# Optimization experiments

Measured on AMD Instinct MI355X. Metric: run time of the kernel, lower is better.

Reference implementation:

```python
import jax, jax.numpy as jnp
import numpy as np

NF, NG, NH, NR, HS = 6, 32, 16, 15, 256
NT, NS = 1000, 2000


def _linear_init(k, fan_in, fan_out):
    s = 1.0 / np.sqrt(fan_in)
    kw, kb = jax.random.split(k)
    W = jax.random.uniform(kw, (fan_in, fan_out), minval=-s, maxval=s, dtype=jnp.float32)
    b = jax.random.uniform(kb, (fan_out,), minval=-s, maxval=s, dtype=jnp.float32)
    return W, b


def setup_inputs() -> dict:
    key = jax.random.key(0)
    ks = jax.random.split(key, 12)
    # forcings: Prcp, Evp, T1(min temp), T2(max temp), Rad, Hum; ensure Prcp>=0 and T2>T1
    base = jax.random.normal(ks[0], (NT, NS)) * 10.0
    spread = jax.random.uniform(ks[1], (NT, NS)) * 5.0 + 0.5
    prcp = jax.random.uniform(ks[2], (NT, NS)) * 10.0
    evp = jax.random.uniform(ks[3], (NT, NS)) * 3.0
    rad = jax.random.uniform(ks[4], (NT, NS))
    hum = jax.random.uniform(ks[5], (NT, NS))
    x = jnp.stack([prcp, evp, base - spread, base + spread, rad, hum], axis=-1).astype(jnp.float32)
    xc = jax.random.normal(ks[6], (NS, NG), dtype=jnp.float32)
    W_fc, b_fc = _linear_init(ks[7], NG, HS)
    W_r, b_r = _linear_init(ks[8], HS, NH * (NR + 1))
    W_g, b_g = _linear_init(ks[9], HS, NH * 9)
    W_kin, b_kin = _linear_init(ks[10], 4, HS)
    W_kout, b_kout = _linear_init(ks[11], HS, NH * 1)
    return dict(x=x, xc=xc, W_fc=W_fc, b_fc=b_fc, W_r=W_r, b_r=b_r,
                W_g=W_g, b_g=b_g, W_kin=W_kin, b_kin=b_kin,
                W_kout=W_kout, b_kout=b_kout)


def reference(x, xc, W_fc, b_fc, W_r, b_r, W_g, b_g, W_kin, b_kin, W_kout, b_kout):
    nt, ns, _ = x.shape
    Prcp, Evp, T1, T2 = x[..., 0], x[..., 1], x[..., 2], x[..., 3]
    f = x[..., 2:]                                   # [nt, ns, 4]

    # --- getParam (eval mode: DropMask is identity) ---
    state = xc @ W_fc + b_fc                         # [ns, hs]
    pK = jnp.tanh(f @ W_kin + b_kin + state) @ W_kout + b_kout   # [nt, ns, nh]
    km = jnp.exp(pK)                                 # melt rate per step
    g = jnp.tanh(state)
    pG = g @ W_g + b_g                               # [ns, 9*nh]
    sl = lambda i: pG[..., i * NH:(i + 1) * NH]
    kp = jax.nn.sigmoid(sl(0))
    ks_ = jax.nn.sigmoid(sl(1))
    kd = jax.nn.sigmoid(sl(2))
    gd = jax.nn.sigmoid(sl(3))
    gl = (jax.nn.sigmoid(sl(4)) * 10.0) ** 3
    qb = jax.nn.relu(sl(5)) / 10.0
    ga = jax.nn.softmax(sl(6), axis=-1)
    gi = jnp.clip(sl(7) / 6.0 + 0.5, 0.0, 1.0) / 2.0   # hardsigmoid/2
    ge = jax.nn.relu(sl(8))

    # one-peak routing weights over nr lags: [nr, ns, nh], sums to 1 over lag
    pR = (g @ W_r + b_r).reshape(ns, NH, NR + 1)
    loc = jax.nn.sigmoid(pR[..., 0]) * NR            # peak location in [0, nr]
    lags = jnp.arange(NR, dtype=x.dtype)
    wR = jax.nn.softmax(pR[..., 1:] - (lags - loc[..., None]) ** 2, axis=-1)
    paramR = jnp.transpose(wR, (2, 0, 1))            # [nr, ns, nh]

    # --- divideP: split precip into snow / liquid by the fraction of [T1,T2] above 0C ---
    vL = jnp.clip(T2 / jnp.maximum(T2 - T1, 1e-6), 0.0, 1.0)
    Pl = (Prcp * vL)[..., None]                      # [nt, ns, 1]
    Ps = (Prcp * (1.0 - vL))[..., None]
    Ev = Evp[..., None]

    # --- bucket.step recurrence over time via scan ---
    def step(carry, inp):
        Sf, Ss, Sd = carry
        ps, pl, ev, kmt = inp
        Sf1 = Sf + ps                                # snow bucket
        qf = jnp.minimum(Sf1, kmt)                   # melt
        Sf2 = Sf1 - qf
        Pin = pl + qf                                # liquid input
        H = jax.nn.relu(Ss + Pin * (1.0 - gi) - ev * ge)   # shallow bucket
        qp = jax.nn.relu(H - gl) * kp                # saturation-excess quick flow
        qo = jnp.minimum(H, gl) * ks_                # shallow drainage
        Ss2 = H - qp - qo
        D = Sd + Pin * gi + qo * gd                  # deep bucket
        qd = D * kd + qb                             # baseflow
        Sd2 = D * (1.0 - kd)
        qTot = qp + qo * (1.0 - gd) + qd             # qp + qs + qd
        return (Sf2, Ss2, Sd2), qTot

    z = jnp.zeros((ns, NH), dtype=x.dtype)
    _, qTot = jax.lax.scan(step, (z, z, z), (Ps, Pl, Ev, km))   # [nt, ns, nh]

    # --- windowed routing convolution + mixture over buckets ---
    # out[j, s] = sum_{i<nr} sum_h qTot[j+i, s, h] * paramR[i, s, h] * ga[s, h]
    W = paramR * ga[None]                            # [nr, ns, nh]
    L = nt - NR + 1
    out = jnp.zeros((L, ns), dtype=x.dtype)
    for i in range(NR):                              # small fixed lag loop
        out = out + jnp.einsum('tsh,sh->ts', qTot[i:i + L], W[i])
    return out
```

## Files before the change

### kernel.cpp

```cpp
#include <hip/hip_runtime.h>
#include <hip/hip_bf16.h>
#include <hip/hip_fp16.h>

#define NG 32
#define NH 16
#define NR 15
#define HS 256
#define NT 1000
#define NS 2000
#define LOUT (NT - NR + 1)
#define TC 40
#define SPB 8
#define NCH (NT / TC)
#define NTP 1001
#define SSB 4

typedef __attribute__((ext_vector_type(8))) short bhalf8;
typedef __attribute__((ext_vector_type(4))) float f32x4;
typedef __attribute__((ext_vector_type(2))) float f32x2;
typedef __attribute__((ext_vector_type(4))) unsigned short us4;
typedef __attribute__((ext_vector_type(8))) unsigned short us8;

__device__ __forceinline__ float fast_rcp(float x) { return __builtin_amdgcn_rcpf(x); }
__device__ __forceinline__ float fast_tanh(float x) {
    float e = __expf(2.0f * x);
    return 1.0f - 2.0f * fast_rcp(e + 1.0f);
}
__device__ __forceinline__ float fast_sigmoid(float x) {
    return fast_rcp(1.0f + __expf(-x));
}
__device__ __forceinline__ short f2bf(float f) {
    __bf16 h = (__bf16)f;
    return __builtin_bit_cast(short, h);
}
__device__ __forceinline__ float h2f(unsigned short u) {
    return (float)__builtin_bit_cast(_Float16, u);
}
__device__ __forceinline__ unsigned short f2h(float f) {
    return __builtin_bit_cast(unsigned short, (_Float16)f);
}

__global__ __launch_bounds__(256) void k_prep(const float* __restrict__ x,
                                              float* __restrict__ xT) {
    int s0 = blockIdx.x * 16;
    int t0 = blockIdx.y * 64;
    int tid = threadIdx.x;
    __shared__ float sX[64][97];
    for (int g = tid; g < 64 * 24; g += 256) {
        int tl = g / 24, c4 = g - tl * 24;
        if (t0 + tl < NT) {
            float4 v = *(const float4*)(x + ((size_t)(t0 + tl) * NS + s0) * 6 + c4 * 4);
            sX[tl][c4 * 4 + 0] = v.x;
            sX[tl][c4 * 4 + 1] = v.y;
            sX[tl][c4 * 4 + 2] = v.z;
            sX[tl][c4 * 4 + 3] = v.w;
        }
    }
    __syncthreads();
    int tl = tid & 63;
    int t = t0 + tl;
    if (t < NT) {
#pragma unroll
        for (int p = 0; p < 4; ++p) {
            int sl = (tid >> 6) + p * 4;
            const float* r = &sX[tl][sl * 6];
            size_t base = ((size_t)(s0 + sl) * 6) * NT + t;
            xT[base + 0 * NT] = r[0];
            xT[base + 1 * NT] = r[1];
            xT[base + 2 * NT] = r[2];
            xT[base + 3 * NT] = r[3];
            xT[base + 4 * NT] = r[4];
            xT[base + 5 * NT] = r[5];
        }
    }
}

__global__ __launch_bounds__(256) void k_site(
    const float* __restrict__ xc, const float* __restrict__ W_fc, const float* __restrict__ b_fc,
    const float* __restrict__ W_r, const float* __restrict__ b_r,
    const float* __restrict__ W_g, const float* __restrict__ b_g,
    const float* __restrict__ b_kin,
    float* __restrict__ state2, float* __restrict__ params, float* __restrict__ wfir)
{
    int s0 = blockIdx.x * SSB, tid = threadIdx.x;
    __shared__ float sXc[SSB][NG];
    __shared__ float sG[SSB][HS];
    __shared__ float sPG[144][SSB];
    __shared__ float sPR[256][SSB];
    if (tid < SSB * NG) sXc[tid >> 5][tid & 31] = xc[(s0 + (tid >> 5)) * NG + (tid & 31)];
    __syncthreads();
    {
        float b = b_fc[tid];
        float a[SSB];
#pragma unroll
        for (int sl = 0; sl < SSB; ++sl) a[sl] = b;
#pragma unroll 8
        for (int g = 0; g < NG; ++g) {
            float w = W_fc[g * HS + tid];
#pragma unroll
            for (int sl = 0; sl < SSB; ++sl) a[sl] += sXc[sl][g] * w;
        }
        float bk = b_kin[tid];
#pragma unroll
        for (int sl = 0; sl < SSB; ++sl) {
            state2[(size_t)(s0 + sl) * HS + tid] = a[sl] + bk;
            sG[sl][tid] = fast_tanh(a[sl]);
        }
    }
    __syncthreads();
    {
        float b = b_r[tid];
        float r[SSB];
#pragma unroll
        for (int sl = 0; sl < SSB; ++sl) r[sl] = b;
#pragma unroll 8
        for (int u = 0; u < HS; ++u) {
            float w = W_r[u * 256 + tid];
#pragma unroll
            for (int sl = 0; sl < SSB; ++sl) r[sl] += sG[sl][u] * w;
        }
#pragma unroll
        for (int sl = 0; sl < SSB; ++sl) sPR[tid][sl] = r[sl];
    }
    if (tid < 144) {
        float b = b_g[tid];
        float gacc[SSB];
#pragma unroll
        for (int sl = 0; sl < SSB; ++sl) gacc[sl] = b;
#pragma unroll 8
        for (int u = 0; u < HS; ++u) {
            float w = W_g[u * 144 + tid];
#pragma unroll
            for (int sl = 0; sl < SSB; ++sl) gacc[sl] += sG[sl][u] * w;
        }
#pragma unroll
        for (int sl = 0; sl < SSB; ++sl) sPG[tid][sl] = gacc[sl];
    }
    __syncthreads();
    if (tid < SSB * NH) {
        int sl = tid >> 4, h = tid & 15;
        int s = s0 + sl;
        float m = -1e30f;
        for (int k = 0; k < NH; ++k) m = fmaxf(m, sPG[96 + k][sl]);
        float sum = 0.f;
        for (int k = 0; k < NH; ++k) sum += __expf(sPG[96 + k][sl] - m);
        float ga = __expf(sPG[96 + h][sl] - m) * fast_rcp(sum);
        float kp = fast_sigmoid(sPG[h][sl]);
        float ks = fast_sigmoid(sPG[16 + h][sl]);
        float kd = fast_sigmoid(sPG[32 + h][sl]);
        float gd = fast_sigmoid(sPG[48 + h][sl]);
        float glv = fast_sigmoid(sPG[64 + h][sl]) * 10.0f;
        float gl = glv * glv * glv;
        float qb = fmaxf(sPG[80 + h][sl], 0.f) * 0.1f;
        float gi = fminf(fmaxf(sPG[112 + h][sl] * (1.0f / 6.0f) + 0.5f, 0.f), 1.f) * 0.5f;
        float ge = fmaxf(sPG[128 + h][sl], 0.f);
        float* P = params + (size_t)s * 128;
        P[0 * 16 + h] = kp;  P[1 * 16 + h] = ks;  P[2 * 16 + h] = kd;  P[3 * 16 + h] = gd;
        P[4 * 16 + h] = gl;  P[5 * 16 + h] = qb;  P[6 * 16 + h] = gi;  P[7 * 16 + h] = ge;
        float loc = fast_sigmoid(sPR[h * 16 + 0][sl]) * 15.0f;
        float l[NR];
        float mm = -1e30f;
#pragma unroll
        for (int i = 0; i < NR; ++i) {
            float d = (float)i - loc;
            l[i] = sPR[h * 16 + 1 + i][sl] - d * d;
            mm = fmaxf(mm, l[i]);
        }
        float ssum = 0.f;
#pragma unroll
        for (int i = 0; i < NR; ++i) { l[i] = __expf(l[i] - mm); ssum += l[i]; }
        float r = fast_rcp(ssum) * ga;
#pragma unroll
        for (int i = 0; i < NR; ++i) wfir[(size_t)s * (NR * NH) + i * NH + h] = l[i] * r;
    }
}

__global__ __launch_bounds__(256) void k_km(
    const float* __restrict__ xT, const float* __restrict__ state2,
    const float* __restrict__ W_kin, const float* __restrict__ W_kout,
    const float* __restrict__ b_kout, _Float16* __restrict__ kmh)
{
    const float Ck = 2.8853900817779268f;
    int s = blockIdx.x, tid = threadIdx.x;
    int wave = tid >> 6, lane = tid & 63;
    int r15 = lane & 15, kg = lane >> 4;

    f32x2 st[2][4], w0[2][4], w1[2][4], w2[2][4], w3[2][4];
    bhalf8 Bf[2];
    float csp = 0.f;
#pragma unroll
    for (int q = 0; q < 2; ++q) {
        int u0 = (2 * wave + q) * 32 + kg * 8;
#pragma unroll
        for (int e = 0; e < 4; ++e) {
            int u = u0 + 2 * e;
            st[q][e] = *(const f32x2*)(state2 + s * HS + u) * Ck;
            w0[q][e] = *(const f32x2*)(W_kin + 0 * HS + u) * Ck;
            w1[q][e] = *(const f32x2*)(W_kin + 1 * HS + u) * Ck;
            w2[q][e] = *(const f32x2*)(W_kin + 2 * HS + u) * Ck;
            w3[q][e] = *(const f32x2*)(W_kin + 3 * HS + u) * Ck;
            float wa = W_kout[(u)     * NH + r15];
            float wb = W_kout[(u + 1) * NH + r15];
            csp += wa + wb;
            Bf[q][2 * e]     = f2bf(-2.0f * wa);
            Bf[q][2 * e + 1] = f2bf(-2.0f * wb);
        }
    }
    __shared__ float sCS[4][4][16];
    sCS[wave][kg][r15] = csp;
    __syncthreads();
    float bk2 = b_kout[r15];
#pragma unroll
    for (int w = 0; w < 4; ++w)
#pragma unroll
        for (int k = 0; k < 4; ++k) bk2 += sCS[w][k][r15];

    const float* fpl = xT + ((size_t)s * 6 + 2) * NT;
    _Float16* kp = kmh + (size_t)s * NT * NH;

    __shared__ f32x4 sRed[2][4][4][64];

    for (int tg = 0; tg < 16; ++tg) {
        int buf = tg & 1;
#pragma unroll
        for (int tile = 0; tile < 4; ++tile) {
            int t = tg * 64 + tile * 16 + r15;
            int tcl = t < NT ? t : NT - 1;
            float f0 = fpl[tcl];
            float f1 = fpl[NT + tcl];
            float f2 = fpl[2 * NT + tcl];
            float f3 = fpl[3 * NT + tcl];
            f32x4 acc = {0.f, 0.f, 0.f, 0.f};
#pragma unroll
            for (int q = 0; q < 2; ++q) {
                bhalf8 A;
#pragma unroll
                for (int e = 0; e < 4; ++e) {
                    f32x2 p = st[q][e];
                    p += f0 * w0[q][e];
                    p += f1 * w1[q][e];
                    p += f2 * w2[q][e];
                    p += f3 * w3[q][e];
                    f32x2 ex = {__builtin_amdgcn_exp2f(p.x), __builtin_amdgcn_exp2f(p.y)};
                    f32x2 e1 = ex + 1.0f;
                    A[2 * e]     = f2bf(fast_rcp(e1.x));
                    A[2 * e + 1] = f2bf(fast_rcp(e1.y));
                }
                acc = __builtin_amdgcn_mfma_f32_16x16x32_bf16(A, Bf[q], acc, 0, 0, 0);
            }
            sRed[buf][tile][wave][lane] = acc;
        }
        __syncthreads();
        {
            f32x4 a0 = sRed[buf][wave][0][lane];
            f32x4 a1 = sRed[buf][wave][1][lane];
            f32x4 a2 = sRed[buf][wave][2][lane];
            f32x4 a3 = sRed[buf][wave][3][lane];
            f32x4 acc = (a0 + a1) + (a2 + a3);
            int tb = tg * 64 + wave * 16;
#pragma unroll
            for (int j = 0; j < 4; ++j) {
                int tt = tb + kg * 4 + j;
                if (tt < NT) kp[(size_t)tt * NH + r15] = (_Float16)__expf(acc[j] + bk2);
            }
        }
    }
}

__global__ __launch_bounds__(128) void k_scan(
    const float* __restrict__ params, const float* __restrict__ xT,
    _Float16* __restrict__ kmh)
{
    int tid = threadIdx.x;
    int sl = tid >> 4, h = tid & 15;
    int S0 = blockIdx.x * SPB;
    __shared__ __align__(16) unsigned short sKmH[2][TC][128];
    __shared__ __align__(16) float sF[2][3][SPB][TC];

    const float* P = params + (size_t)(S0 + sl) * 128;
    float kp = P[h], ks = P[16 + h], kd = P[32 + h], gd = P[48 + h];
    float gl = P[64 + h], qb = P[80 + h], gi = P[96 + h], ge = P[112 + h];
    float gi1 = 1.f - gi, gd1 = 1.f - gd, kd1 = 1.f - kd;
    float Sf = 0.f, Ss = 0.f, Sd = 0.f;

    us4 vkm[10];
    float4 fP, fE, fT1, fT2;
    int fsite = tid / 10, ftcq = tid - fsite * 10;
    size_t fbase = ((size_t)(S0 + (fsite < SPB ? fsite : 0)) * 6) * NT + ftcq * 4;

    auto LOAD = [&](int t0) {
#pragma unroll
        for (int r = 0; r < 10; ++r) {
            int g = r * 128 + tid;
            int site = g / 160;
            int rem = g - site * 160;
            int tc = rem >> 2, h0 = (rem & 3) << 2;
            vkm[r] = *(const us4*)(kmh + (((size_t)(S0 + site) * NT + t0 + tc) * NH + h0));
        }
        if (tid < 80) {
            fP  = *(const float4*)(xT + fbase + t0);
            fE  = *(const float4*)(xT + fbase + (size_t)NT + t0);
            fT1 = *(const float4*)(xT + fbase + 2 * (size_t)NT + t0);
            fT2 = *(const float4*)(xT + fbase + 3 * (size_t)NT + t0);
        }
    };
    auto STORE_LDS = [&](int b) {
#pragma unroll
        for (int r = 0; r < 10; ++r) {
            int g = r * 128 + tid;
            int site = g / 160;
            int rem = g - site * 160;
            int tc = rem >> 2, h0 = (rem & 3) << 2;
            *(us4*)&sKmH[b][tc][site * 16 + h0] = vkm[r];
        }
        if (tid < 80) {
            float4 ps, pl;
            {
                float den = fmaxf(fT2.x - fT1.x, 1e-6f);
                float vL = fminf(fmaxf(fT2.x * fast_rcp(den), 0.f), 1.f);
                pl.x = fP.x * vL; ps.x = fP.x - pl.x;
            }
            {
                float den = fmaxf(fT2.y - fT1.y, 1e-6f);
                float vL = fminf(fmaxf(fT2.y * fast_rcp(den), 0.f), 1.f);
                pl.y = fP.y * vL; ps.y = fP.y - pl.y;
            }
            {
                float den = fmaxf(fT2.z - fT1.z, 1e-6f);
                float vL = fminf(fmaxf(fT2.z * fast_rcp(den), 0.f), 1.f);
                pl.z = fP.z * vL; ps.z = fP.z - pl.z;
            }
            {
                float den = fmaxf(fT2.w - fT1.w, 1e-6f);
                float vL = fminf(fmaxf(fT2.w * fast_rcp(den), 0.f), 1.f);
                pl.w = fP.w * vL; ps.w = fP.w - pl.w;
            }
            *(float4*)&sF[b][0][fsite][ftcq * 4] = ps;
            *(float4*)&sF[b][1][fsite][ftcq * 4] = pl;
            *(float4*)&sF[b][2][fsite][ftcq * 4] = fE;
        }
    };

    size_t qbase = ((size_t)(S0 + sl) * NT) * NH + h;

    LOAD(0);
    STORE_LDS(0);
    __syncthreads();
    for (int c = 0; c < NCH; ++c) {
        int b = c & 1;
        if (c + 1 < NCH) LOAD((c + 1) * TC);
        int t0 = c * TC;
#pragma unroll 8
        for (int tc = 0; tc < TC; ++tc) {
            float ps = sF[b][0][sl][tc], pl = sF[b][1][sl][tc], ev = sF[b][2][sl][tc];
            float kmv = h2f(sKmH[b][tc][tid]);
            Sf += ps;
            float qf = fminf(Sf, kmv);
            Sf -= qf;
            float Pin = pl + qf;
            float H = fmaxf(Ss + Pin * gi1 - ev * ge, 0.f);
            float qp = fmaxf(H - gl, 0.f) * kp;
            float qo = fminf(H, gl) * ks;
            Ss = H - qp - qo;
            float D = Sd + Pin * gi + qo * gd;
            float qd = D * kd + qb;
            Sd = D * kd1;
            kmh[qbase + (size_t)(t0 + tc) * NH] = (_Float16)(qp + qo * gd1 + qd);
        }
        if (c + 1 < NCH) {
            STORE_LDS((c + 1) & 1);
            __syncthreads();
        }
    }
}

__global__ __launch_bounds__(256) void k_fir(
    const _Float16* __restrict__ kmh, const float* __restrict__ wfir,
    float* __restrict__ out)
{
    int s = blockIdx.x, tid = threadIdx.x;
    __shared__ float sQ[NH * NTP];
    __shared__ float sW[NR * NH];
    const us8* src = (const us8*)(kmh + (size_t)s * NT * NH);
    for (int g = tid; g < NT * NH / 8; g += 256) {
        us8 v = src[g];
        int t = g >> 1, h0 = (g & 1) << 3;
#pragma unroll
        for (int e = 0; e < 8; ++e)
            sQ[(h0 + e) * NTP + t] = h2f(v[e]);
    }
    if (tid < NR * NH) sW[tid] = wfir[(size_t)s * NR * NH + tid];
    __syncthreads();
#pragma unroll
    for (int c = 0; c < 4; ++c) {
        int tau = tid + 256 * c;
        if (tau < LOUT) {
            float acc = 0.f;
#pragma unroll
            for (int hh = 0; hh < NH; ++hh) {
                const float* q = sQ + hh * NTP + tau;
#pragma unroll
                for (int i = 0; i < NR; ++i) acc += q[i] * sW[i * 16 + hh];
            }
            out[(size_t)tau * NS + s] = acc;
        }
    }
}

extern "C" void kernel_launch(void* const* d_in, const int* in_sizes, int n_in,
                              void* d_out, int out_size, void* d_ws, size_t ws_size,
                              hipStream_t stream) {
    const float* x      = (const float*)d_in[0];
    const float* xc     = (const float*)d_in[1];
    const float* W_fc   = (const float*)d_in[2];
    const float* b_fc   = (const float*)d_in[3];
    const float* W_r    = (const float*)d_in[4];
    const float* b_r    = (const float*)d_in[5];
    const float* W_g    = (const float*)d_in[6];
    const float* b_g    = (const float*)d_in[7];
    const float* W_kin  = (const float*)d_in[8];
    const float* b_kin  = (const float*)d_in[9];
    const float* W_kout = (const float*)d_in[10];
    const float* b_kout = (const float*)d_in[11];
    float* out = (float*)d_out;

    float* ws     = (float*)d_ws;
    float* state2 = ws;
    float* params = state2 + (size_t)NS * HS;
    float* wfir   = params + (size_t)NS * 128;
    float* xT     = wfir + (size_t)NS * NR * NH;
    _Float16* kmh = (_Float16*)(xT + (size_t)NS * 6 * NT);

    k_prep<<<dim3(NS / 16, (NT + 63) / 64), 256, 0, stream>>>(x, xT);
    k_site<<<NS / SSB, 256, 0, stream>>>(xc, W_fc, b_fc, W_r, b_r, W_g, b_g, b_kin,
                                         state2, params, wfir);
    k_km<<<NS, 256, 0, stream>>>(xT, state2, W_kin, W_kout, b_kout, kmh);
    k_scan<<<NS / SPB, 128, 0, stream>>>(params, xT, kmh);
    k_fir<<<NS, 256, 0, stream>>>(kmh, wfir, out);
}
```

Before: 315.1 us.

## Register-block FIR over four outputs with fp16 LDS staging in k_fir

The routing convolution kernel now keeps the staged qTot in LDS as raw fp16 (half the footprint) and transposes the weights to per-bucket rows. Each thread computes four consecutive output times, loading a 20-sample window with vector LDS reads and reusing each sample across the 15 taps. This cuts LDS traffic per FMA, and the smaller LDS footprint may allow more resident blocks. In exchange, only about 250 of the 256 threads are active and the stores per thread are strided by NS.

After: 285.6 us (median of 2 runs). -9.4%, faster.

```diff
diff --git a/kernel.cpp b/kernel.cpp
--- a/kernel.cpp
+++ b/kernel.cpp
@@ -12,8 +12,8 @@
 #define TC 40
 #define SPB 8
 #define NCH (NT / TC)
-#define NTP 1001
 #define SSB 4
+#define QROW 1048
 
 typedef __attribute__((ext_vector_type(8))) short bhalf8;
 typedef __attribute__((ext_vector_type(4))) float f32x4;
@@ -379,31 +379,49 @@
     float* __restrict__ out)
 {
     int s = blockIdx.x, tid = threadIdx.x;
-    __shared__ float sQ[NH * NTP];
-    __shared__ float sW[NR * NH];
+    __shared__ unsigned short sQ[NH][QROW];
+    __shared__ float sW[NH][16];
+    for (int idx = tid; idx < NH * (QROW - NT); idx += 256) {
+        int h = idx / (QROW - NT), j = idx - h * (QROW - NT);
+        sQ[h][NT + j] = 0;
+    }
     const us8* src = (const us8*)(kmh + (size_t)s * NT * NH);
     for (int g = tid; g < NT * NH / 8; g += 256) {
         us8 v = src[g];
         int t = g >> 1, h0 = (g & 1) << 3;
 #pragma unroll
-        for (int e = 0; e < 8; ++e)
-            sQ[(h0 + e) * NTP + t] = h2f(v[e]);
-    }
-    if (tid < NR * NH) sW[tid] = wfir[(size_t)s * NR * NH + tid];
-    __syncthreads();
-#pragma unroll
-    for (int c = 0; c < 4; ++c) {
-        int tau = tid + 256 * c;
-        if (tau < LOUT) {
-            float acc = 0.f;
-#pragma unroll
-            for (int hh = 0; hh < NH; ++hh) {
-                const float* q = sQ + hh * NTP + tau;
-#pragma unroll
-                for (int i = 0; i < NR; ++i) acc += q[i] * sW[i * 16 + hh];
-            }
-            out[(size_t)tau * NS + s] = acc;
-        }
+        for (int e = 0; e < 8; ++e) sQ[h0 + e][t] = v[e];
+    }
+    if (tid < NR * NH) sW[tid & 15][tid >> 4] = wfir[(size_t)s * NR * NH + tid];
+    __syncthreads();
+
+    int tau0 = tid * 4;
+    if (tau0 < LOUT) {
+        float a0 = 0.f, a1 = 0.f, a2 = 0.f, a3 = 0.f;
+#pragma unroll 1
+        for (int h = 0; h < NH; ++h) {
+            float q[20];
+#pragma unroll
+            for (int r = 0; r < 5; ++r) {
+                us4 v = *(const us4*)&sQ[h][tau0 + 4 * r];
+                q[4 * r + 0] = h2f(v[0]);
+                q[4 * r + 1] = h2f(v[1]);
+                q[4 * r + 2] = h2f(v[2]);
+                q[4 * r + 3] = h2f(v[3]);
+            }
+#pragma unroll
+            for (int i = 0; i < NR; ++i) {
+                float w = sW[h][i];
+                a0 += q[i] * w;
+                a1 += q[i + 1] * w;
+                a2 += q[i + 2] * w;
+                a3 += q[i + 3] * w;
+            }
+        }
+        out[(size_t)(tau0 + 0) * NS + s] = a0;
+        if (tau0 + 1 < LOUT) out[(size_t)(tau0 + 1) * NS + s] = a1;
+        if (tau0 + 2 < LOUT) out[(size_t)(tau0 + 2) * NS + s] = a2;
+        if (tau0 + 3 < LOUT) out[(size_t)(tau0 + 3) * NS + s] = a3;
     }
 }
 
```
